# Kernel tuning notes

Measured on AMD Instinct MI355X. Metric: run time of the kernel, lower is better.

## Reference

```python
import jax, jax.numpy as jnp
import numpy as np

D_MODEL = 1024
NUM_HEADS = 16
D_HEAD = D_MODEL // NUM_HEADS
LN_EPS = 1e-5
ROPE_BASE = 10000.0


def layer_norm(x, w, b=None, eps=LN_EPS):
    mu = jnp.mean(x, axis=-1, keepdims=True)
    var = jnp.mean(jnp.square(x - mu), axis=-1, keepdims=True)
    y = (x - mu) * jax.lax.rsqrt(var + eps) * w
    return y + b if b is not None else y


def _rotate_half(x):
    x1, x2 = jnp.split(x, 2, axis=-1)
    return jnp.concatenate([-x2, x1], axis=-1)


def apply_rotary(q, k):
    # q, k: [B, S, H, Dh]
    s, dh = q.shape[1], q.shape[-1]
    inv_freq = 1.0 / (ROPE_BASE ** (jnp.arange(0, dh, 2, dtype=jnp.float32) / dh))
    t = jnp.arange(s, dtype=jnp.float32)
    freqs = jnp.outer(t, inv_freq)                      # [S, Dh/2]
    emb = jnp.concatenate([freqs, freqs], axis=-1)      # [S, Dh]
    cos = jnp.cos(emb)[None, :, None, :].astype(q.dtype)
    sin = jnp.sin(emb)[None, :, None, :].astype(q.dtype)
    q_rot = q * cos + _rotate_half(q) * sin
    k_rot = k * cos + _rotate_half(k) * sin
    return q_rot, k_rot


def setup_inputs() -> dict:
    key = jax.random.key(0)
    ks = jax.random.split(key, 8)
    B, L, D = 4, 2048, D_MODEL
    x = jax.random.normal(ks[0], (B, L, D), dtype=jnp.float32)
    sequence_id = jnp.sort(jax.random.randint(ks[1], (B, L), 0, 8), axis=-1).astype(jnp.int64)
    scale = 1.0 / np.sqrt(D)
    return {
        "x": x,
        "sequence_id": sequence_id,
        "ln_w": jnp.ones((D,), jnp.float32),
        "ln_b": jnp.zeros((D,), jnp.float32),
        "w_qkv": jax.random.normal(ks[2], (D, 3 * D), jnp.float32) * scale,
        "q_ln_w": jnp.ones((D,), jnp.float32),
        "k_ln_w": jnp.ones((D,), jnp.float32),
        "w_out": jax.random.normal(ks[3], (D, D), jnp.float32) * scale,
    }


def reference(x, sequence_id, ln_w, ln_b, w_qkv, q_ln_w, k_ln_w, w_out):
    B, L, D = x.shape
    H, Dh = NUM_HEADS, D_HEAD
    # fused LayerNorm + QKV projection
    qkv = layer_norm(x, ln_w, ln_b) @ w_qkv              # [B, L, 3D]
    q, k, v = jnp.split(qkv, 3, axis=-1)
    # qk layernorm (scale only, bias=False)
    q = layer_norm(q, q_ln_w)
    k = layer_norm(k, k_ln_w)
    # split heads and apply rotary
    q = q.reshape(B, L, H, Dh)
    k = k.reshape(B, L, H, Dh)
    q, k = apply_rotary(q, k)
    v = v.reshape(B, L, H, Dh)
    # packed-sequence mask: tokens attend only within same sequence id
    mask = (sequence_id[:, :, None] == sequence_id[:, None, :])[:, None, :, :]  # [B,1,L,L]
    scale = 1.0 / np.sqrt(Dh)
    scores = jnp.einsum("bqhd,bkhd->bhqk", q, k) * scale
    scores = jnp.where(mask, scores, jnp.finfo(scores.dtype).min)
    attn = jax.nn.softmax(scores, axis=-1)
    ctx = jnp.einsum("bhqk,bkhd->bqhd", attn, v).reshape(B, L, D)
    return ctx @ w_out
```

## Files before the change

### kernel.cpp

```cpp
#include <hip/hip_runtime.h>
#include <hip/hip_bf16.h>
#include <cstdint>
#include <cstddef>
#include <type_traits>

#define D_MODEL 1024
#define NH      16
#define DH      64
#define LSEQ    2048
#define BATCH   4
#define NTOK    8192
#define K3      3072

typedef __attribute__((ext_vector_type(8))) short  short8;
typedef __attribute__((ext_vector_type(4))) float  floatx4;

__device__ __forceinline__ unsigned short f2bf_bits(float f) {
  __hip_bfloat16 h = __float2bfloat16(f);
  return __builtin_bit_cast(unsigned short, h);
}
__device__ __forceinline__ float bf2f(unsigned short u) {
  return __bfloat162float(__builtin_bit_cast(__hip_bfloat16, u));
}
__device__ __forceinline__ unsigned int pack_bf16(float lo, float hi) {
  return (unsigned int)f2bf_bits(lo) | ((unsigned int)f2bf_bits(hi) << 16);
}

__device__ __forceinline__ void gld_lds16(const void* g, void* l) {
  __builtin_amdgcn_global_load_lds(
      (const __attribute__((address_space(1))) void*)g,
      (__attribute__((address_space(3))) void*)l,
      16, 0, 0);
}

__global__ __launch_bounds__(256)
void prep_kernel(const float* __restrict__ x, const float* __restrict__ ln_w,
                 const float* __restrict__ ln_b, const float* __restrict__ w_qkv,
                 const float* __restrict__ w_out, const int* __restrict__ sid,
                 __hip_bfloat16* __restrict__ hbuf, __hip_bfloat16* __restrict__ wqkvT,
                 __hip_bfloat16* __restrict__ woutT, int* __restrict__ segstart,
                 int* __restrict__ segend) {
  __shared__ __align__(16) char smem[8448];
  const int blk = blockIdx.x;
  const int tid = threadIdx.x;

  if (blk < 4096) {
    float (*tile)[33] = reinterpret_cast<float(*)[33]>(smem);
    const float* src;  __hip_bfloat16* dst;  int R, C, bx, by;
    if (blk < 3072) { src = w_qkv; dst = wqkvT; R = 1024; C = 3072; bx = blk % 96; by = blk / 96; }
    else            { src = w_out; dst = woutT; R = 1024; C = 1024; bx = (blk - 3072) & 31; by = (blk - 3072) >> 5; }
    const int c0 = bx * 32, r0 = by * 32;
    const int xx = tid & 31, yy = tid >> 5;
    #pragma unroll
    for (int j = 0; j < 32; j += 8)
      tile[yy + j][xx] = src[(size_t)(r0 + yy + j) * C + c0 + xx];
    __syncthreads();
    #pragma unroll
    for (int j = 0; j < 32; j += 8)
      dst[(size_t)(c0 + yy + j) * R + r0 + xx] = __float2bfloat16(tile[xx][yy + j]);
  } else if (blk < 6144) {
    const int lane = tid & 63;
    const int t = (blk - 4096) * 4 + (tid >> 6);
    const float4* xr = reinterpret_cast<const float4*>(x) + (size_t)t * 256;
    float4 v[4];
    float s = 0.f, ss = 0.f;
    #pragma unroll
    for (int i = 0; i < 4; i++) {
      v[i] = xr[lane + i * 64];
      s  += (v[i].x + v[i].y) + (v[i].z + v[i].w);
      ss += (v[i].x*v[i].x + v[i].y*v[i].y) + (v[i].z*v[i].z + v[i].w*v[i].w);
    }
    #pragma unroll
    for (int off = 1; off < 64; off <<= 1) {
      s  += __shfl_xor(s, off);
      ss += __shfl_xor(ss, off);
    }
    const float mu = s * (1.f / 1024);
    const float rs = rsqrtf(ss * (1.f / 1024) - mu * mu + 1e-5f);
    const float4* wr = reinterpret_cast<const float4*>(ln_w);
    const float4* br = reinterpret_cast<const float4*>(ln_b);
    ushort4* hr = reinterpret_cast<ushort4*>(hbuf) + (size_t)t * 256;
    #pragma unroll
    for (int i = 0; i < 4; i++) {
      const float4 wv = wr[lane + i * 64];
      const float4 bv = br[lane + i * 64];
      ushort4 o;
      o.x = f2bf_bits((v[i].x - mu) * rs * wv.x + bv.x);
      o.y = f2bf_bits((v[i].y - mu) * rs * wv.y + bv.y);
      o.z = f2bf_bits((v[i].z - mu) * rs * wv.z + bv.z);
      o.w = f2bf_bits((v[i].w - mu) * rs * wv.w + bv.w);
      hr[lane + i * 64] = o;
    }
  } else {
    int* srow = reinterpret_cast<int*>(smem);
    const int sblk = blk - 6144;
    const int b = sblk >> 3;
    const int* row = sid + (size_t)b * LSEQ;
    #pragma unroll
    for (int i = 0; i < 8; i++) srow[tid + i * 256] = row[tid + i * 256];
    __syncthreads();
    const int l = (sblk & 7) * 256 + tid;
    const int v = srow[l];
    int lo = 0, hi = l;
    while (lo < hi) { int mid = (lo + hi) >> 1; if (srow[mid] < v) lo = mid + 1; else hi = mid; }
    const int i = b * LSEQ + l;
    segstart[i] = lo;
    lo = l + 1; hi = LSEQ;
    while (lo < hi) { int mid = (lo + hi) >> 1; if (srow[mid] <= v) lo = mid + 1; else hi = mid; }
    segend[i] = lo;
  }
}

template <typename OutT>
__global__ __launch_bounds__(256, 2)
void gemm_bt(const __hip_bfloat16* __restrict__ A, const __hip_bfloat16* __restrict__ Bt,
             OutT* __restrict__ C, int M, int N, int K) {
  const int tid  = threadIdx.x;
  const int lane = tid & 63;
  const int wave = tid >> 6;
  const int bm = blockIdx.y * 128;
  const int bn = blockIdx.x * 128;
  const int wm = (wave & 1) * 64;
  const int wn = (wave >> 1) * 64;
  const int quad = lane >> 4;
  const int l16  = lane & 15;

  __shared__ __align__(16) __hip_bfloat16 As[128 * 64];
  __shared__ __align__(16) __hip_bfloat16 Bs[128 * 64];

  floatx4 acc[4][4];
  #pragma unroll
  for (int i = 0; i < 4; i++)
    #pragma unroll
    for (int j = 0; j < 4; j++) {
      floatx4 z = {0.f, 0.f, 0.f, 0.f};
      acc[i][j] = z;
    }

  const int srow = tid >> 3;
  const int sq   = tid & 7;
  const int sc8  = (sq ^ (srow & 7)) * 8;
  const __hip_bfloat16* Ab = A  + (size_t)(bm + srow) * K + sc8;
  const __hip_bfloat16* Bb = Bt + (size_t)(bn + srow) * K + sc8;

  const int axr = l16 & 7;

  for (int k0 = 0; k0 < K; k0 += 64) {
    __syncthreads();
    #pragma unroll
    for (int p = 0; p < 4; p++) {
      gld_lds16(Ab + (size_t)(p * 32) * K + k0, (char*)As + p * 4096 + tid * 16);
      gld_lds16(Bb + (size_t)(p * 32) * K + k0, (char*)Bs + p * 4096 + tid * 16);
    }
    __syncthreads();
    #pragma unroll
    for (int s0 = 0; s0 < 2; s0++) {
      const int qo = ((s0 * 4 + quad) ^ axr) * 8;
      short8 af[4], bfr[4];
      #pragma unroll
      for (int i = 0; i < 4; i++)
        af[i] = *reinterpret_cast<const short8*>(As + (wm + i * 16 + l16) * 64 + qo);
      #pragma unroll
      for (int j = 0; j < 4; j++)
        bfr[j] = *reinterpret_cast<const short8*>(Bs + (wn + j * 16 + l16) * 64 + qo);
      #pragma unroll
      for (int i = 0; i < 4; i++)
        #pragma unroll
        for (int j = 0; j < 4; j++)
          acc[i][j] = __builtin_amdgcn_mfma_f32_16x16x32_bf16(af[i], bfr[j], acc[i][j], 0, 0, 0);
    }
  }

  #pragma unroll
  for (int i = 0; i < 4; i++)
    #pragma unroll
    for (int j = 0; j < 4; j++) {
      const int row0 = bm + wm + i * 16 + quad * 4;
      const int col  = bn + wn + j * 16 + l16;
      #pragma unroll
      for (int r = 0; r < 4; r++) {
        if constexpr (std::is_same<OutT, __hip_bfloat16>::value)
          C[(size_t)(row0 + r) * N + col] = __float2bfloat16(acc[i][j][r]);
        else
          C[(size_t)(row0 + r) * N + col] = acc[i][j][r];
      }
    }
}

__global__ __launch_bounds__(256)
void ropevt_kernel(const unsigned short* __restrict__ qkv, const float* __restrict__ qw,
                   const float* __restrict__ kw, unsigned short* __restrict__ qT,
                   unsigned short* __restrict__ kT, unsigned short* __restrict__ vT) {
  __shared__ __align__(16) unsigned short T[64 * 64];
  const int blk = blockIdx.x;
  const int tid = threadIdx.x;

  if (blk < 2048) {
    const int lane = tid & 63;
    const int t = blk * 4 + (tid >> 6);
    const int b = t >> 11, l = t & 2047;
    const unsigned short* row = qkv + (size_t)t * K3;
    const int hh = lane >> 2;
    const int jb = (lane & 3) * 8;
    const int base = hh * 64 + jb;

    const short8 qa_u = *reinterpret_cast<const short8*>(row + base);
    const short8 qb_u = *reinterpret_cast<const short8*>(row + base + 32);
    const short8 ka_u = *reinterpret_cast<const short8*>(row + 1024 + base);
    const short8 kb_u = *reinterpret_cast<const short8*>(row + 1024 + base + 32);

    float qa[8], qb[8], ka[8], kb[8];
    float s_q = 0.f, ss_q = 0.f, s_k = 0.f, ss_k = 0.f;
    #pragma unroll
    for (int e = 0; e < 8; e++) {
      qa[e] = bf2f((unsigned short)qa_u[e]); qb[e] = bf2f((unsigned short)qb_u[e]);
      ka[e] = bf2f((unsigned short)ka_u[e]); kb[e] = bf2f((unsigned short)kb_u[e]);
      s_q  += qa[e] + qb[e];  ss_q += qa[e]*qa[e] + qb[e]*qb[e];
      s_k  += ka[e] + kb[e];  ss_k += ka[e]*ka[e] + kb[e]*kb[e];
    }
    #pragma unroll
    for (int off = 1; off < 64; off <<= 1) {
      s_q  += __shfl_xor(s_q, off);  ss_q += __shfl_xor(ss_q, off);
      s_k  += __shfl_xor(s_k, off);  ss_k += __shfl_xor(ss_k, off);
    }
    const float qmu = s_q * (1.f/1024);
    const float qrs = rsqrtf(ss_q * (1.f/1024) - qmu*qmu + 1e-5f);
    const float kmu = s_k * (1.f/1024);
    const float krs = rsqrtf(ss_k * (1.f/1024) - kmu*kmu + 1e-5f);

    const int j0 = lane & 31;
    const float invf = __expf(-(float)j0 * 0.28782313662425575f);
    float tsin, tcos;
    sincosf((float)l * invf, &tsin, &tcos);

    const float4 wq0 = *reinterpret_cast<const float4*>(qw + base);
    const float4 wq1 = *reinterpret_cast<const float4*>(qw + base + 4);
    const float4 wq2 = *reinterpret_cast<const float4*>(qw + base + 32);
    const float4 wq3 = *reinterpret_cast<const float4*>(qw + base + 36);
    const float4 wk0 = *reinterpret_cast<const float4*>(kw + base);
    const float4 wk1 = *reinterpret_cast<const float4*>(kw + base + 4);
    const float4 wk2 = *reinterpret_cast<const float4*>(kw + base + 32);
    const float4 wk3 = *reinterpret_cast<const float4*>(kw + base + 36);
    const float wqa[8] = {wq0.x,wq0.y,wq0.z,wq0.w, wq1.x,wq1.y,wq1.z,wq1.w};
    const float wqb[8] = {wq2.x,wq2.y,wq2.z,wq2.w, wq3.x,wq3.y,wq3.z,wq3.w};
    const float wka[8] = {wk0.x,wk0.y,wk0.z,wk0.w, wk1.x,wk1.y,wk1.z,wk1.w};
    const float wkb[8] = {wk2.x,wk2.y,wk2.z,wk2.w, wk3.x,wk3.y,wk3.z,wk3.w};

    short8 oqa, oqb, oka, okb;
    #pragma unroll
    for (int e = 0; e < 8; e++) {
      const int j = jb + e;
      const float c  = __shfl(tcos, j);
      const float sn = __shfl(tsin, j);
      const float qn1 = (qa[e] - qmu) * qrs * wqa[e];
      const float qn2 = (qb[e] - qmu) * qrs * wqb[e];
      const float kn1 = (ka[e] - kmu) * krs * wka[e];
      const float kn2 = (kb[e] - kmu) * krs * wkb[e];
      oqa[e] = (short)f2bf_bits((qn1 * c - qn2 * sn) * 0.125f);
      oqb[e] = (short)f2bf_bits((qn2 * c + qn1 * sn) * 0.125f);
      oka[e] = (short)f2bf_bits(kn1 * c - kn2 * sn);
      okb[e] = (short)f2bf_bits(kn2 * c + kn1 * sn);
    }
    const size_t ob = ((size_t)(b * NH + hh) * LSEQ + l) * DH + jb;
    *reinterpret_cast<short8*>(qT + ob)      = oqa;
    *reinterpret_cast<short8*>(qT + ob + 32) = oqb;
    *reinterpret_cast<short8*>(kT + ob)      = oka;
    *reinterpret_cast<short8*>(kT + ob + 32) = okb;
  } else {
    const int blkv = blk - 2048;
    const int l0 = (blkv & 31) * 64;
    const int bh = blkv >> 5;
    const int b = bh >> 4, h = bh & 15;
    const int sr = tid >> 3, scc = tid & 7;
    const int r1 = sr + 32;
    gld_lds16(qkv + (size_t)(b * LSEQ + l0 + sr) * K3 + 2048 + h * 64 + ((scc ^ ((sr >> 3) & 7)) * 8),
              (char*)T + tid * 16);
    gld_lds16(qkv + (size_t)(b * LSEQ + l0 + r1) * K3 + 2048 + h * 64 + ((scc ^ ((r1 >> 3) & 7)) * 8),
              (char*)T + 4096 + tid * 16);
    __syncthreads();
    #pragma unroll
    for (int it = 0; it < 2; it++) {
      const int cid = tid + it * 256;
      const int dh = cid >> 3, c = (cid & 7) * 8;
      const int sl = (dh >> 3) ^ ((c >> 3) & 7);
      short8 o;
      #pragma unroll
      for (int e = 0; e < 8; e++)
        o[e] = (short)T[(c + e) * 64 + sl * 8 + (dh & 7)];
      *reinterpret_cast<short8*>(vT + ((size_t)bh * DH + dh) * LSEQ + l0 + c) = o;
    }
  }
}

__global__ __launch_bounds__(256, 2)
void attn_mfma(const unsigned short* __restrict__ qT, const unsigned short* __restrict__ kT,
               const unsigned short* __restrict__ vT, const int* __restrict__ segs,
               const int* __restrict__ sege, unsigned short* __restrict__ ctx) {
  const int tid  = threadIdx.x;
  const int lane = tid & 63, w = tid >> 6;
  const int quad = lane >> 4, l16 = lane & 15;

  const int fid = blockIdx.x + (blockIdx.y << 4) + (blockIdx.z << 8);
  const int sw  = (fid & 7) * 128 + (fid >> 3);
  const int qbase = (sw & 15) * 128;
  const int h = (sw >> 4) & 15, b = sw >> 8;

  const size_t bh = (size_t)(b * NH + h);
  const unsigned short* Kg = kT + bh * LSEQ * DH;
  const unsigned short* Vg = vT + bh * DH * LSEQ;

  __shared__ __align__(16) unsigned short Ps[4][32 * 72];

  short8 qf[2][2];
  int st[2], en[2], gmin[2], gmax[2];
  #pragma unroll
  for (int g = 0; g < 2; g++) {
    const int qy = qbase + w * 32 + g * 16 + l16;
    const unsigned short* Qrow = qT + (bh * LSEQ + qy) * DH;
    qf[g][0] = *reinterpret_cast<const short8*>(Qrow + quad * 8);
    qf[g][1] = *reinterpret_cast<const short8*>(Qrow + 32 + quad * 8);
    st[g] = segs[b * LSEQ + qy];
    en[g] = sege[b * LSEQ + qy];
    gmin[g] = segs[b * LSEQ + qbase + w * 32 + g * 16];
    gmax[g] = sege[b * LSEQ + qbase + w * 32 + g * 16 + 15];
  }
  const int wstart = gmin[0] & ~63;
  const int wmax   = gmax[1];

  floatx4 acc[2][4];
  #pragma unroll
  for (int g = 0; g < 2; g++)
    #pragma unroll
    for (int dt = 0; dt < 4; dt++) { floatx4 z = {0.f,0.f,0.f,0.f}; acc[g][dt] = z; }
  float m[2] = {-1e30f, -1e30f}, lsum[2] = {0.f, 0.f};

  short8 kf[4][2];
  #pragma unroll
  for (int t = 0; t < 4; t++) {
    const unsigned short* kp = Kg + (size_t)(wstart + t * 16 + l16) * DH + quad * 8;
    kf[t][0] = *reinterpret_cast<const short8*>(kp);
    kf[t][1] = *reinterpret_cast<const short8*>(kp + 32);
  }

  for (int kk = wstart; kk < wmax; kk += 64) {
    const bool have_next = (kk + 64) < wmax;

    short8 kn[4][2];
    if (have_next) {
      #pragma unroll
      for (int t = 0; t < 4; t++) {
        const unsigned short* kp = Kg + (size_t)(kk + 64 + t * 16 + l16) * DH + quad * 8;
        kn[t][0] = *reinterpret_cast<const short8*>(kp);
        kn[t][1] = *reinterpret_cast<const short8*>(kp + 32);
      }
    }

    bool act[2];
    float alpha[2];
    #pragma unroll
    for (int g = 0; g < 2; g++) {
      act[g] = !(kk + 64 <= gmin[g] || kk >= gmax[g]);
      alpha[g] = 1.f;
    }

    floatx4 sc[2][4];
    #pragma unroll
    for (int t = 0; t < 4; t++) {
      #pragma unroll
      for (int g = 0; g < 2; g++) {
        if (!act[g]) continue;
        floatx4 z = {0.f,0.f,0.f,0.f};
        sc[g][t] = __builtin_amdgcn_mfma_f32_16x16x32_bf16(kf[t][0], qf[g][0], z, 0, 0, 0);
        sc[g][t] = __builtin_amdgcn_mfma_f32_16x16x32_bf16(kf[t][1], qf[g][1], sc[g][t], 0, 0, 0);
      }
    }

    short8 vf[4][2];
    #pragma unroll
    for (int dt = 0; dt < 4; dt++) {
      const unsigned short* vp = Vg + (size_t)(dt * 16 + l16) * LSEQ + kk + quad * 8;
      vf[dt][0] = *reinterpret_cast<const short8*>(vp);
      vf[dt][1] = *reinterpret_cast<const short8*>(vp + 32);
    }

    #pragma unroll
    for (int g = 0; g < 2; g++) {
      if (!act[g]) continue;
      const unsigned span = (unsigned)(en[g] - st[g]);
      float vm = -1e30f;
      #pragma unroll
      for (int t = 0; t < 4; t++) {
        const int k0 = kk + t * 16 + quad * 4;
        #pragma unroll
        for (int r = 0; r < 4; r++) {
          const bool ok = (unsigned)(k0 + r - st[g]) < span;
          sc[g][t][r] = ok ? sc[g][t][r] : -1e30f;
          vm = fmaxf(vm, sc[g][t][r]);
        }
      }
      vm = fmaxf(vm, __shfl_xor(vm, 16));
      vm = fmaxf(vm, __shfl_xor(vm, 32));
      const float mn = fmaxf(fmaxf(m[g], vm), -20.f);
      alpha[g] = __expf(m[g] - mn);
      m[g] = mn;

      float rs = 0.f;
      #pragma unroll
      for (int t = 0; t < 4; t++) {
        const float p0 = __expf(sc[g][t][0] - mn);
        const float p1 = __expf(sc[g][t][1] - mn);
        const float p2 = __expf(sc[g][t][2] - mn);
        const float p3 = __expf(sc[g][t][3] - mn);
        rs += (p0 + p1) + (p2 + p3);
        uint2 pk;
        pk.x = pack_bf16(p0, p1);
        pk.y = pack_bf16(p2, p3);
        *reinterpret_cast<uint2*>(&Ps[w][(g * 16 + l16) * 72 + t * 16 + quad * 4]) = pk;
      }
      rs += __shfl_xor(rs, 16);
      rs += __shfl_xor(rs, 32);
      lsum[g] = lsum[g] * alpha[g] + rs;
    }

    short8 pf[2][2];
    #pragma unroll
    for (int g = 0; g < 2; g++) {
      if (!act[g]) continue;
      pf[g][0] = *reinterpret_cast<const short8*>(&Ps[w][(g * 16 + l16) * 72 + quad * 8]);
      pf[g][1] = *reinterpret_cast<const short8*>(&Ps[w][(g * 16 + l16) * 72 + 32 + quad * 8]);
    }
    #pragma unroll
    for (int dt = 0; dt < 4; dt++) {
      #pragma unroll
      for (int g = 0; g < 2; g++) {
        if (!act[g]) continue;
        #pragma unroll
        for (int r = 0; r < 4; r++) acc[g][dt][r] *= alpha[g];
        acc[g][dt] = __builtin_amdgcn_mfma_f32_16x16x32_bf16(vf[dt][0], pf[g][0], acc[g][dt], 0, 0, 0);
        acc[g][dt] = __builtin_amdgcn_mfma_f32_16x16x32_bf16(vf[dt][1], pf[g][1], acc[g][dt], 0, 0, 0);
      }
    }

    if (have_next) {
      #pragma unroll
      for (int t = 0; t < 4; t++) {
        kf[t][0] = kn[t][0];
        kf[t][1] = kn[t][1];
      }
    }
  }

  #pragma unroll
  for (int g = 0; g < 2; g++) {
    const float inv = (lsum[g] > 0.f) ? 1.f / lsum[g] : 0.f;
    const int qy = qbase + w * 32 + g * 16 + l16;
    unsigned short* orow = ctx + ((size_t)(b * LSEQ + qy)) * D_MODEL + h * DH;
    #pragma unroll
    for (int dt = 0; dt < 4; dt++) {
      uint2 o;
      o.x = pack_bf16(acc[g][dt][0] * inv, acc[g][dt][1] * inv);
      o.y = pack_bf16(acc[g][dt][2] * inv, acc[g][dt][3] * inv);
      *reinterpret_cast<uint2*>(orow + dt * 16 + quad * 4) = o;
    }
  }
}

extern "C" void kernel_launch(void* const* d_in, const int* in_sizes, int n_in,
                              void* d_out, int out_size, void* d_ws, size_t ws_size,
                              hipStream_t stream) {
  const float* x      = (const float*)d_in[0];
  const int*   sid    = (const int*)d_in[1];
  const float* ln_w   = (const float*)d_in[2];
  const float* ln_b   = (const float*)d_in[3];
  const float* w_qkv  = (const float*)d_in[4];
  const float* q_ln_w = (const float*)d_in[5];
  const float* k_ln_w = (const float*)d_in[6];
  const float* w_out  = (const float*)d_in[7];
  float* out = (float*)d_out;
  char* ws = (char*)d_ws;

  constexpr size_t OFF_WQKVT = 0;
  constexpr size_t OFF_WOUTT = 6291456;
  constexpr size_t OFF_H     = 8388608;
  constexpr size_t OFF_QKV   = 25165824;
  constexpr size_t OFF_QT    = 75497472;
  constexpr size_t OFF_KT    = 92274688;
  constexpr size_t OFF_VT    = 109051904;
  constexpr size_t OFF_CTX   = 125829120;
  constexpr size_t OFF_SEGS  = 142606336;
  constexpr size_t OFF_SEGE  = 142639104;

  __hip_bfloat16* wqkvT = (__hip_bfloat16*)(ws + OFF_WQKVT);
  __hip_bfloat16* woutT = (__hip_bfloat16*)(ws + OFF_WOUTT);
  __hip_bfloat16* hbuf  = (__hip_bfloat16*)(ws + OFF_H);
  __hip_bfloat16* qkvb  = (__hip_bfloat16*)(ws + OFF_QKV);
  unsigned short* qTb   = (unsigned short*)(ws + OFF_QT);
  unsigned short* kTb   = (unsigned short*)(ws + OFF_KT);
  unsigned short* vTb   = (unsigned short*)(ws + OFF_VT);
  unsigned short* ctx   = (unsigned short*)(ws + OFF_CTX);
  int*            segst = (int*)(ws + OFF_SEGS);
  int*            segen = (int*)(ws + OFF_SEGE);

  prep_kernel<<<6176, 256, 0, stream>>>(x, ln_w, ln_b, w_qkv, w_out, sid,
                                        hbuf, wqkvT, woutT, segst, segen);
  gemm_bt<__hip_bfloat16><<<dim3(K3 / 128, NTOK / 128), 256, 0, stream>>>(
      hbuf, wqkvT, qkvb, NTOK, K3, 1024);
  ropevt_kernel<<<4096, 256, 0, stream>>>((const unsigned short*)qkvb, q_ln_w, k_ln_w,
                                          qTb, kTb, vTb);
  attn_mfma<<<dim3(LSEQ / 128, NH, BATCH), 256, 0, stream>>>(qTb, kTb, vTb, segst, segen, ctx);
  gemm_bt<float><<<dim3(D_MODEL / 128, NTOK / 128), 256, 0, stream>>>(
      (const __hip_bfloat16*)ctx, woutT, out, NTOK, D_MODEL, 1024);
}
```

Before: 259.1 us.

## Use lazy softmax rescaling, hoist V loads, and prioritize MFMA in attention

Measured after the change: 254.6 us. About the same (-1.8%).

```diff
diff --git a/kernel.cpp b/kernel.cpp
--- a/kernel.cpp
+++ b/kernel.cpp
@@ -332,7 +332,8 @@
   for (int g = 0; g < 2; g++)
     #pragma unroll
     for (int dt = 0; dt < 4; dt++) { floatx4 z = {0.f,0.f,0.f,0.f}; acc[g][dt] = z; }
-  float m[2] = {-1e30f, -1e30f}, lsum[2] = {0.f, 0.f};
+  float m[2] = {9.f, 9.f};
+  float lsum[2] = {0.f, 0.f};
 
   short8 kf[4][2];
   #pragma unroll
@@ -345,6 +346,13 @@
   for (int kk = wstart; kk < wmax; kk += 64) {
     const bool have_next = (kk + 64) < wmax;
 
+    short8 vf[4][2];
+    #pragma unroll
+    for (int dt = 0; dt < 4; dt++) {
+      const unsigned short* vp = Vg + (size_t)(dt * 16 + l16) * LSEQ + kk + quad * 8;
+      vf[dt][0] = *reinterpret_cast<const short8*>(vp);
+      vf[dt][1] = *reinterpret_cast<const short8*>(vp + 32);
+    }
     short8 kn[4][2];
     if (have_next) {
       #pragma unroll
@@ -356,36 +364,24 @@
     }
 
     bool act[2];
-    float alpha[2];
-    #pragma unroll
-    for (int g = 0; g < 2; g++) {
+    #pragma unroll
+    for (int g = 0; g < 2; g++)
       act[g] = !(kk + 64 <= gmin[g] || kk >= gmax[g]);
-      alpha[g] = 1.f;
-    }
-
-    floatx4 sc[2][4];
-    #pragma unroll
-    for (int t = 0; t < 4; t++) {
-      #pragma unroll
-      for (int g = 0; g < 2; g++) {
-        if (!act[g]) continue;
-        floatx4 z = {0.f,0.f,0.f,0.f};
-        sc[g][t] = __builtin_amdgcn_mfma_f32_16x16x32_bf16(kf[t][0], qf[g][0], z, 0, 0, 0);
-        sc[g][t] = __builtin_amdgcn_mfma_f32_16x16x32_bf16(kf[t][1], qf[g][1], sc[g][t], 0, 0, 0);
-      }
-    }
-
-    short8 vf[4][2];
-    #pragma unroll
-    for (int dt = 0; dt < 4; dt++) {
-      const unsigned short* vp = Vg + (size_t)(dt * 16 + l16) * LSEQ + kk + quad * 8;
-      vf[dt][0] = *reinterpret_cast<const short8*>(vp);
-      vf[dt][1] = *reinterpret_cast<const short8*>(vp + 32);
-    }
 
     #pragma unroll
     for (int g = 0; g < 2; g++) {
       if (!act[g]) continue;
+
+      floatx4 sc[4];
+      __builtin_amdgcn_s_setprio(1);
+      #pragma unroll
+      for (int t = 0; t < 4; t++) {
+        floatx4 z = {0.f,0.f,0.f,0.f};
+        sc[t] = __builtin_amdgcn_mfma_f32_16x16x32_bf16(kf[t][0], qf[g][0], z, 0, 0, 0);
+        sc[t] = __builtin_amdgcn_mfma_f32_16x16x32_bf16(kf[t][1], qf[g][1], sc[t], 0, 0, 0);
+      }
+      __builtin_amdgcn_s_setprio(0);
+
       const unsigned span = (unsigned)(en[g] - st[g]);
       float vm = -1e30f;
       #pragma unroll
@@ -394,32 +390,38 @@
         #pragma unroll
         for (int r = 0; r < 4; r++) {
           const bool ok = (unsigned)(k0 + r - st[g]) < span;
-          sc[g][t][r] = ok ? sc[g][t][r] : -1e30f;
-          vm = fmaxf(vm, sc[g][t][r]);
+          sc[t][r] = ok ? sc[t][r] : -1e30f;
+          vm = fmaxf(vm, sc[t][r]);
         }
       }
-      vm = fmaxf(vm, __shfl_xor(vm, 16));
-      vm = fmaxf(vm, __shfl_xor(vm, 32));
-      const float mn = fmaxf(fmaxf(m[g], vm), -20.f);
-      alpha[g] = __expf(m[g] - mn);
-      m[g] = mn;
-
+
+      if (__any(vm > m[g])) {
+        float vv = fmaxf(vm, __shfl_xor(vm, 16));
+        vv = fmaxf(vv, __shfl_xor(vv, 32));
+        const float a = __expf(m[g] - vv);
+        lsum[g] *= a;
+        #pragma unroll
+        for (int dt = 0; dt < 4; dt++)
+          #pragma unroll
+          for (int r = 0; r < 4; r++) acc[g][dt][r] *= a;
+        m[g] = vv;
+      }
+
+      const float mn = m[g];
       float rs = 0.f;
       #pragma unroll
       for (int t = 0; t < 4; t++) {
-        const float p0 = __expf(sc[g][t][0] - mn);
-        const float p1 = __expf(sc[g][t][1] - mn);
-        const float p2 = __expf(sc[g][t][2] - mn);
-        const float p3 = __expf(sc[g][t][3] - mn);
+        const float p0 = __expf(sc[t][0] - mn);
+        const float p1 = __expf(sc[t][1] - mn);
+        const float p2 = __expf(sc[t][2] - mn);
+        const float p3 = __expf(sc[t][3] - mn);
         rs += (p0 + p1) + (p2 + p3);
         uint2 pk;
         pk.x = pack_bf16(p0, p1);
         pk.y = pack_bf16(p2, p3);
         *reinterpret_cast<uint2*>(&Ps[w][(g * 16 + l16) * 72 + t * 16 + quad * 4]) = pk;
       }
-      rs += __shfl_xor(rs, 16);
-      rs += __shfl_xor(rs, 32);
-      lsum[g] = lsum[g] * alpha[g] + rs;
+      lsum[g] += rs;
     }
 
     short8 pf[2][2];
@@ -429,17 +431,17 @@
       pf[g][0] = *reinterpret_cast<const short8*>(&Ps[w][(g * 16 + l16) * 72 + quad * 8]);
       pf[g][1] = *reinterpret_cast<const short8*>(&Ps[w][(g * 16 + l16) * 72 + 32 + quad * 8]);
     }
+    __builtin_amdgcn_s_setprio(1);
     #pragma unroll
     for (int dt = 0; dt < 4; dt++) {
       #pragma unroll
       for (int g = 0; g < 2; g++) {
         if (!act[g]) continue;
-        #pragma unroll
-        for (int r = 0; r < 4; r++) acc[g][dt][r] *= alpha[g];
         acc[g][dt] = __builtin_amdgcn_mfma_f32_16x16x32_bf16(vf[dt][0], pf[g][0], acc[g][dt], 0, 0, 0);
         acc[g][dt] = __builtin_amdgcn_mfma_f32_16x16x32_bf16(vf[dt][1], pf[g][1], acc[g][dt], 0, 0, 0);
       }
     }
+    __builtin_amdgcn_s_setprio(0);
 
     if (have_next) {
       #pragma unroll
@@ -452,6 +454,8 @@
 
   #pragma unroll
   for (int g = 0; g < 2; g++) {
+    lsum[g] += __shfl_xor(lsum[g], 16);
+    lsum[g] += __shfl_xor(lsum[g], 32);
     const float inv = (lsum[g] > 0.f) ? 1.f / lsum[g] : 0.f;
     const int qy = qbase + w * 32 + g * 16 + l16;
     unsigned short* orow = ctx + ((size_t)(b * LSEQ + qy)) * D_MODEL + h * DH;
```
